# Kernel optimization log

Hardware: AMD Instinct MI355X
Metric: run time of the kernel (lower is better)

## Reference

```python
import jax, jax.numpy as jnp
import numpy as np

D_MODEL = 1024
NUM_HEADS = 16
MAX_SEQ_LEN = 2048
BATCH = 4
SEQ_LEN = 2048


def setup_inputs() -> dict:
    key = jax.random.key(0)
    ks = jax.random.split(key, 7)
    s = 0.02
    return {
        "x": jax.random.normal(ks[0], (BATCH, SEQ_LEN, D_MODEL), dtype=jnp.float32),
        "Wq": jax.random.normal(ks[1], (D_MODEL, D_MODEL), dtype=jnp.float32) * s,
        "Wk": jax.random.normal(ks[2], (D_MODEL, D_MODEL), dtype=jnp.float32) * s,
        "Wv": jax.random.normal(ks[3], (D_MODEL, D_MODEL), dtype=jnp.float32) * s,
        "Wo": jax.random.normal(ks[4], (D_MODEL, D_MODEL), dtype=jnp.float32) * s,
        "bo": jnp.zeros((D_MODEL,), dtype=jnp.float32),
        "bias_table": jax.random.normal(ks[5], (2 * MAX_SEQ_LEN - 1, NUM_HEADS), dtype=jnp.float32) * s,
    }


def reference(x, Wq, Wk, Wv, Wo, bo, bias_table):
    B, S, D = x.shape
    H = NUM_HEADS
    hd = D // H
    scale = hd ** -0.5

    # torch Linear: y = x @ W.T
    q = (x @ Wq.T).reshape(B, S, H, hd).transpose(0, 2, 1, 3)  # [B,H,S,hd]
    k = (x @ Wk.T).reshape(B, S, H, hd).transpose(0, 2, 1, 3)
    v = (x @ Wv.T).reshape(B, S, H, hd).transpose(0, 2, 1, 3)

    scores = jnp.einsum("bhqd,bhkd->bhqk", q, k) * scale  # [B,H,S,S]

    # relative index: coords[:,None] - coords[None,:] + max_seq_len - 1
    coords = jnp.arange(S)
    rel_idx = coords[:, None] - coords[None, :] + MAX_SEQ_LEN - 1  # [S,S]
    rel_bias = bias_table[rel_idx]              # [S,S,H]
    rel_bias = rel_bias.transpose(2, 0, 1)[None]  # [1,H,S,S]

    probs = jax.nn.softmax(scores + rel_bias, axis=-1)
    ctx = jnp.einsum("bhqk,bhkd->bhqd", probs, v)  # [B,H,S,hd]
    ctx = ctx.transpose(0, 2, 1, 3).reshape(B, S, D)
    return ctx @ Wo.T + bo
```

## Files before the change

### kernel.cpp

```cpp
#include <hip/hip_runtime.h>
#include <string.h>

typedef unsigned short u16;
typedef unsigned int   u32;
typedef __attribute__((ext_vector_type(8))) short short8;
typedef __attribute__((ext_vector_type(4))) float f32x4;
typedef __attribute__((ext_vector_type(16))) float f32x16;
typedef __attribute__((ext_vector_type(2))) __fp16 h2;
typedef __attribute__((ext_vector_type(8))) __fp16 h8;
typedef __attribute__((ext_vector_type(2))) unsigned int u32x2;

__device__ __forceinline__ u16 f2b(float f) {
  u32 u = __float_as_uint(f);
  u32 r = (u + 0x7fffu + ((u >> 16) & 1u)) >> 16;
  return (u16)r;
}
__device__ __forceinline__ void cp16(const u16* g, u16* l) {
  __builtin_amdgcn_global_load_lds(
      (const __attribute__((address_space(1))) void*)g,
      (__attribute__((address_space(3))) void*)l, 16, 0, 0);
}
__device__ __forceinline__ void plswap(u32& a, u32& b) {
  u32x2 r = __builtin_amdgcn_permlane32_swap(a, b, false, false);
  a = r[0]; b = r[1];
}

__global__ __launch_bounds__(256) void cvt_f2b_kernel(const float* __restrict__ in,
                                                      u16* __restrict__ out, int n) {
  int i = (blockIdx.x * 256 + threadIdx.x) * 4;
  if (i + 3 < n) {
    float4 v = *(const float4*)&in[i];
    ushort4 o = make_ushort4(f2b(v.x), f2b(v.y), f2b(v.z), f2b(v.w));
    *(ushort4*)&out[i] = o;
  }
}
__global__ __launch_bounds__(256) void cvtw_kernel(const float* __restrict__ w0,
                                                   const float* __restrict__ w1,
                                                   const float* __restrict__ w2,
                                                   const float* __restrict__ w3,
                                                   u16* __restrict__ out) {
  const float* src = (blockIdx.y == 0) ? w0 : (blockIdx.y == 1) ? w1
                   : (blockIdx.y == 2) ? w2 : w3;
  int i = (blockIdx.x * 256 + threadIdx.x) * 4;
  float4 v = *(const float4*)&src[i];
  ushort4 o = make_ushort4(f2b(v.x), f2b(v.y), f2b(v.z), f2b(v.w));
  *(ushort4*)&out[(size_t)blockIdx.y * 1048576 + i] = o;
}

template<int MODE>
__global__ __launch_bounds__(256) void gemm128_bt(
    const u16* __restrict__ A, const u16* __restrict__ Bw,
    void* __restrict__ outp, const float* __restrict__ bias,
    const int M, const int N, const int K) {
  __shared__ __attribute__((aligned(16))) u16 As[2][128 * 32];
  __shared__ __attribute__((aligned(16))) u16 Bs[2][128 * 32];

  const u16* Bw2 = Bw;
  if (MODE == 0) Bw2 += ((size_t)blockIdx.z) << 20;

  const int tid  = threadIdx.x;
  const int wave = tid >> 6, lane = tid & 63;
  const int quad = lane >> 4, l15 = lane & 15;
  const int wm   = (wave >> 1) * 64, wn = (wave & 1) * 64;
  const int m0   = blockIdx.x * 128, n0 = blockIdx.y * 128;

  const int srow = wave * 32 + (lane >> 2);
  const int scol = (lane & 3) * 8;
  const u16* gA0 = A   + (size_t)(m0 + srow) * K + scol;
  const u16* gA1 = gA0 + (size_t)16 * K;
  const u16* gB0 = Bw2 + (size_t)(n0 + srow) * K + scol;
  const u16* gB1 = gB0 + (size_t)16 * K;
  const int lo0 = (wave * 32) * 32, lo1 = (wave * 32 + 16) * 32;

  cp16(gA0, &As[0][lo0]); cp16(gA1, &As[0][lo1]);
  cp16(gB0, &Bs[0][lo0]); cp16(gB1, &Bs[0][lo1]);
  gA0 += 32; gA1 += 32; gB0 += 32; gB1 += 32;

  f32x4 acc[4][4] = {};
  const int nk = K >> 5;
  for (int kt = 0; kt < nk; ++kt) {
    const int cur = kt & 1;
    __syncthreads();
    if (kt + 1 < nk) {
      cp16(gA0, &As[1 - cur][lo0]); cp16(gA1, &As[1 - cur][lo1]);
      cp16(gB0, &Bs[1 - cur][lo0]); cp16(gB1, &Bs[1 - cur][lo1]);
      gA0 += 32; gA1 += 32; gB0 += 32; gB1 += 32;
    }
    short8 af[4], bf[4];
    #pragma unroll
    for (int mi = 0; mi < 4; ++mi)
      af[mi] = *(const short8*)&As[cur][(wm + mi * 16 + l15) * 32 + quad * 8];
    #pragma unroll
    for (int ni = 0; ni < 4; ++ni)
      bf[ni] = *(const short8*)&Bs[cur][(wn + ni * 16 + l15) * 32 + quad * 8];
    #pragma unroll
    for (int mi = 0; mi < 4; ++mi)
      #pragma unroll
      for (int ni = 0; ni < 4; ++ni)
        acc[mi][ni] = __builtin_amdgcn_mfma_f32_16x16x32_bf16(af[mi], bf[ni], acc[mi][ni], 0, 0, 0);
  }

  #pragma unroll
  for (int mi = 0; mi < 4; ++mi)
    #pragma unroll
    for (int ni = 0; ni < 4; ++ni) {
      if (MODE == 0 && blockIdx.z == 2) {
        int mb = m0 + wm + mi * 16 + quad * 4;
        int n  = n0 + wn + ni * 16 + l15;
        int b = mb >> 11, s = mb & 2047, h = n >> 6, d = n & 63;
        u16* out = (u16*)outp + (((size_t)2) << 23);
        h2 p0 = __builtin_amdgcn_cvt_pkrtz(acc[mi][ni][0], acc[mi][ni][1]);
        h2 p1 = __builtin_amdgcn_cvt_pkrtz(acc[mi][ni][2], acc[mi][ni][3]);
        ushort4 o;
        memcpy(&o.x, &p0, 4);
        memcpy(&o.z, &p1, 4);
        *(ushort4*)&out[((((size_t)b * 16 + h) * 64 + d) << 11) + s] = o;
      } else {
        #pragma unroll
        for (int r = 0; r < 4; ++r) {
          int m = m0 + wm + mi * 16 + quad * 4 + r;
          int n = n0 + wn + ni * 16 + l15;
          float v = acc[mi][ni][r];
          if (MODE == 0) {
            int b = m >> 11, s = m & 2047, h = n >> 6, d = n & 63;
            u16* out = (u16*)outp + (((size_t)blockIdx.z) << 23);
            out[((((size_t)b * 16 + h) * 2048 + s) << 6) + d] = f2b(v);
          } else {
            ((float*)outp)[(size_t)m * N + n] = v + bias[n];
          }
        }
      }
    }
}

__global__ __launch_bounds__(256, 4) void attn_mfma_kernel(
    const u16* __restrict__ qb, const u16* __restrict__ kb, const u16* __restrict__ vtb,
    const float* __restrict__ bias_table, u16* __restrict__ ctx) {
  __shared__ __attribute__((aligned(16))) u16 Ks[2][64 * 64];
  __shared__ __attribute__((aligned(16))) u16 Vs[64 * 64];
  __shared__ __attribute__((aligned(16))) float bias_s[2304];

  const int tid  = threadIdx.x;
  const int wave = tid >> 6, lane = tid & 63;
  const int l31  = lane & 31, hi = lane >> 5;
  const int xsw  = l31 & 7;
  const int bh   = blockIdx.x, h = bh & 15, b = bh >> 4;
  const int q0   = blockIdx.y * 128;

  for (int i = tid; i < 2175; i += 256)
    bias_s[i] = bias_table[(q0 + i) * 16 + h] * 1.44269504f;

  short8 aQ[4];
  #pragma unroll
  for (int ks = 0; ks < 4; ++ks)
    aQ[ks] = *(const short8*)&qb[((size_t)bh * 2048 + q0 + wave * 32 + l31) * 64
                                 + ks * 16 + hi * 8];

  f32x16 accO[2] = {};
  float  lsum = 0.f;

  const int krow = lane >> 3;
  const int kchk = (lane & 7) ^ krow;
  const u16* kbase = kb + (((size_t)bh * 2048) << 6);

  const int srow = tid >> 2, t0 = tid & 3, ssw = srow & 7;
  const u16* vrow = vtb + (((size_t)bh * 64 + srow) << 11) + t0 * 16;
  const int vo0 = srow * 64 + (((2 * t0    ) ^ ssw) << 3);
  const int vo1 = srow * 64 + (((2 * t0 + 1) ^ ssw) << 3);

  short8 vpre0 = *(const short8*)&vrow[0];
  short8 vpre1 = *(const short8*)&vrow[8];
  #pragma unroll
  for (int g = 0; g < 2; ++g)
    cp16(kbase + (size_t)(wave * 16 + g * 8 + krow) * 64 + kchk * 8,
         &Ks[0][(wave * 16 + g * 8) * 64]);

  for (int kt = 0; kt < 32; ++kt) {
    const int cur = kt & 1;
    __syncthreads();
    *(short8*)&Vs[vo0] = vpre0;
    *(short8*)&Vs[vo1] = vpre1;
    __syncthreads();
    if (kt < 31) {
      const u16* vp = vrow + ((size_t)(kt + 1) << 6);
      vpre0 = *(const short8*)&vp[0];
      vpre1 = *(const short8*)&vp[8];
      #pragma unroll
      for (int g = 0; g < 2; ++g)
        cp16(kbase + (size_t)((kt + 1) * 64 + wave * 16 + g * 8 + krow) * 64 + kchk * 8,
             &Ks[1 - cur][(wave * 16 + g * 8) * 64]);
    }

    #pragma unroll
    for (int t = 0; t < 2; ++t) {
      f32x16 accS = {};
      #pragma unroll
      for (int ks = 0; ks < 4; ++ks) {
        short8 aK = *(const short8*)&Ks[cur][(t * 32 + l31) * 64
                                            + (((ks * 2 + hi) ^ xsw) << 3)];
        accS = __builtin_amdgcn_mfma_f32_32x32x16_bf16(aK, aQ[ks], accS, 0, 0, 0);
      }

      u32 d[8];
      const int ib = wave * 32 + l31 - kt * 64 - t * 32 - 4 * hi + 2047;
      #pragma unroll
      for (int rg = 0; rg < 4; ++rg) {
        const int bb = ib - 8 * rg;
        float p0 = __builtin_amdgcn_exp2f(fmaf(accS[4 * rg + 0], 0.18033688f, bias_s[bb    ]));
        float p1 = __builtin_amdgcn_exp2f(fmaf(accS[4 * rg + 1], 0.18033688f, bias_s[bb - 1]));
        float p2 = __builtin_amdgcn_exp2f(fmaf(accS[4 * rg + 2], 0.18033688f, bias_s[bb - 2]));
        float p3 = __builtin_amdgcn_exp2f(fmaf(accS[4 * rg + 3], 0.18033688f, bias_s[bb - 3]));
        lsum += (p0 + p1) + (p2 + p3);
        h2 e0; e0[0] = (__fp16)p0; e0[1] = (__fp16)p1;
        h2 e1; e1[0] = (__fp16)p2; e1[1] = (__fp16)p3;
        memcpy(&d[2 * rg],     &e0, 4);
        memcpy(&d[2 * rg + 1], &e1, 4);
      }

      #pragma unroll
      for (int sl = 0; sl < 2; ++sl) {
        u32 F0 = d[4 * sl], F1 = d[4 * sl + 1], F2 = d[4 * sl + 2], F3 = d[4 * sl + 3];
        plswap(F0, F2);
        plswap(F1, F3);
        union { u32 w[4]; h8 v; } uf;
        uf.w[0] = F0; uf.w[1] = F1; uf.w[2] = F2; uf.w[3] = F3;
        const int ch = ((t * 2 + sl) * 2 + hi) ^ xsw;
        #pragma unroll
        for (int dt = 0; dt < 2; ++dt) {
          short8 av = *(const short8*)&Vs[(dt * 32 + l31) * 64 + (ch << 3)];
          h8 avh; memcpy(&avh, &av, 16);
          accO[dt] = __builtin_amdgcn_mfma_f32_32x32x16_f16(avh, uf.v, accO[dt], 0, 0, 0);
        }
      }
    }
  }

  const float ltot = lsum + __shfl_xor(lsum, 32);
  const float inv  = 1.0f / ltot;
  const int q = q0 + wave * 32 + l31;
  #pragma unroll
  for (int dt = 0; dt < 2; ++dt)
    #pragma unroll
    for (int rg = 0; rg < 4; ++rg) {
      ushort4 o = make_ushort4(f2b(accO[dt][4 * rg + 0] * inv), f2b(accO[dt][4 * rg + 1] * inv),
                               f2b(accO[dt][4 * rg + 2] * inv), f2b(accO[dt][4 * rg + 3] * inv));
      *(ushort4*)&ctx[((size_t)b * 2048 + q) * 1024 + h * 64 + dt * 32 + rg * 8 + hi * 4] = o;
    }
}

extern "C" void kernel_launch(void* const* d_in, const int* in_sizes, int n_in,
                              void* d_out, int out_size, void* d_ws, size_t ws_size,
                              hipStream_t stream) {
  const float* x          = (const float*)d_in[0];
  const float* Wq         = (const float*)d_in[1];
  const float* Wk         = (const float*)d_in[2];
  const float* Wv         = (const float*)d_in[3];
  const float* Wo         = (const float*)d_in[4];
  const float* bo         = (const float*)d_in[5];
  const float* bias_table = (const float*)d_in[6];
  float* out = (float*)d_out;

  char* ws = (char*)d_ws;
  u16* xb   = (u16*)(ws);
  u16* wqb  = (u16*)(ws + 16777216);
  u16* wob  = (u16*)(ws + 16777216 + 3 * 2097152);
  u16* qb   = (u16*)(ws + 25165824);
  u16* kb   = qb + 8388608;
  u16* vtb  = kb + 8388608;
  u16* ctxb = (u16*)(ws + 75497472);

  cvt_f2b_kernel<<<8192, 256, 0, stream>>>(x, xb, 8388608);
  cvtw_kernel<<<dim3(1024, 4), 256, 0, stream>>>(Wq, Wk, Wv, Wo, wqb);

  gemm128_bt<0><<<dim3(64, 8, 3), 256, 0, stream>>>(
      xb, wqb, (void*)qb, nullptr, 8192, 1024, 1024);

  attn_mfma_kernel<<<dim3(64, 16), 256, 0, stream>>>(qb, kb, vtb, bias_table, ctxb);

  gemm128_bt<1><<<dim3(64, 8), 256, 0, stream>>>(
      ctxb, wob, (void*)out, bo, 8192, 1024, 1024);
}
```

Baseline: 293.4 us.

## Process two Q sub-tiles per wave and double-buffer V in attention

Each wave now handles 64 query rows (two 32-row sub-tiles) instead of 32, so every K and V fragment read from LDS feeds twice as many MFMAs and the block covers 256 queries. V is double-buffered in shared memory, which removes one __syncthreads per key tile, and its global prefetch is moved two tiles ahead. The cost is more registers (launch bounds lowered from 4 to 2 blocks per SM) and half as many blocks (512), which may reduce occupancy and latency hiding.

After: 276.0 us. -5.9%, faster.

```diff
diff --git a/kernel.cpp b/kernel.cpp
--- a/kernel.cpp
+++ b/kernel.cpp
@@ -133,11 +133,11 @@
     }
 }
 
-__global__ __launch_bounds__(256, 4) void attn_mfma_kernel(
+__global__ __launch_bounds__(256, 2) void attn_mfma_kernel(
     const u16* __restrict__ qb, const u16* __restrict__ kb, const u16* __restrict__ vtb,
     const float* __restrict__ bias_table, u16* __restrict__ ctx) {
   __shared__ __attribute__((aligned(16))) u16 Ks[2][64 * 64];
-  __shared__ __attribute__((aligned(16))) u16 Vs[64 * 64];
+  __shared__ __attribute__((aligned(16))) u16 Vs[2][64 * 64];
   __shared__ __attribute__((aligned(16))) float bias_s[2304];
 
   const int tid  = threadIdx.x;
@@ -145,19 +145,21 @@
   const int l31  = lane & 31, hi = lane >> 5;
   const int xsw  = l31 & 7;
   const int bh   = blockIdx.x, h = bh & 15, b = bh >> 4;
-  const int q0   = blockIdx.y * 128;
-
-  for (int i = tid; i < 2175; i += 256)
+  const int q0   = blockIdx.y * 256;
+
+  for (int i = tid; i < 2303; i += 256)
     bias_s[i] = bias_table[(q0 + i) * 16 + h] * 1.44269504f;
 
-  short8 aQ[4];
+  short8 aQ[2][4];
   #pragma unroll
-  for (int ks = 0; ks < 4; ++ks)
-    aQ[ks] = *(const short8*)&qb[((size_t)bh * 2048 + q0 + wave * 32 + l31) * 64
-                                 + ks * 16 + hi * 8];
-
-  f32x16 accO[2] = {};
-  float  lsum = 0.f;
+  for (int qs = 0; qs < 2; ++qs)
+    #pragma unroll
+    for (int ks = 0; ks < 4; ++ks)
+      aQ[qs][ks] = *(const short8*)&qb[((size_t)bh * 2048 + q0 + wave * 64 + qs * 32 + l31) * 64
+                                       + ks * 16 + hi * 8];
+
+  f32x16 accO[2][2] = {};
+  float  lsum[2] = {0.f, 0.f};
 
   const int krow = lane >> 3;
   const int kchk = (lane & 7) ^ krow;
@@ -170,82 +172,102 @@
 
   short8 vpre0 = *(const short8*)&vrow[0];
   short8 vpre1 = *(const short8*)&vrow[8];
+  *(short8*)&Vs[0][vo0] = vpre0;
+  *(short8*)&Vs[0][vo1] = vpre1;
   #pragma unroll
   for (int g = 0; g < 2; ++g)
     cp16(kbase + (size_t)(wave * 16 + g * 8 + krow) * 64 + kchk * 8,
          &Ks[0][(wave * 16 + g * 8) * 64]);
+  vpre0 = *(const short8*)&vrow[64];
+  vpre1 = *(const short8*)&vrow[72];
 
   for (int kt = 0; kt < 32; ++kt) {
     const int cur = kt & 1;
     __syncthreads();
-    *(short8*)&Vs[vo0] = vpre0;
-    *(short8*)&Vs[vo1] = vpre1;
-    __syncthreads();
     if (kt < 31) {
-      const u16* vp = vrow + ((size_t)(kt + 1) << 6);
-      vpre0 = *(const short8*)&vp[0];
-      vpre1 = *(const short8*)&vp[8];
       #pragma unroll
       for (int g = 0; g < 2; ++g)
         cp16(kbase + (size_t)((kt + 1) * 64 + wave * 16 + g * 8 + krow) * 64 + kchk * 8,
              &Ks[1 - cur][(wave * 16 + g * 8) * 64]);
+      *(short8*)&Vs[1 - cur][vo0] = vpre0;
+      *(short8*)&Vs[1 - cur][vo1] = vpre1;
+      if (kt < 30) {
+        const u16* vp = vrow + ((size_t)(kt + 2) << 6);
+        vpre0 = *(const short8*)&vp[0];
+        vpre1 = *(const short8*)&vp[8];
+      }
     }
 
     #pragma unroll
     for (int t = 0; t < 2; ++t) {
-      f32x16 accS = {};
-      #pragma unroll
-      for (int ks = 0; ks < 4; ++ks) {
-        short8 aK = *(const short8*)&Ks[cur][(t * 32 + l31) * 64
-                                            + (((ks * 2 + hi) ^ xsw) << 3)];
-        accS = __builtin_amdgcn_mfma_f32_32x32x16_bf16(aK, aQ[ks], accS, 0, 0, 0);
-      }
-
-      u32 d[8];
-      const int ib = wave * 32 + l31 - kt * 64 - t * 32 - 4 * hi + 2047;
-      #pragma unroll
-      for (int rg = 0; rg < 4; ++rg) {
-        const int bb = ib - 8 * rg;
-        float p0 = __builtin_amdgcn_exp2f(fmaf(accS[4 * rg + 0], 0.18033688f, bias_s[bb    ]));
-        float p1 = __builtin_amdgcn_exp2f(fmaf(accS[4 * rg + 1], 0.18033688f, bias_s[bb - 1]));
-        float p2 = __builtin_amdgcn_exp2f(fmaf(accS[4 * rg + 2], 0.18033688f, bias_s[bb - 2]));
-        float p3 = __builtin_amdgcn_exp2f(fmaf(accS[4 * rg + 3], 0.18033688f, bias_s[bb - 3]));
-        lsum += (p0 + p1) + (p2 + p3);
-        h2 e0; e0[0] = (__fp16)p0; e0[1] = (__fp16)p1;
-        h2 e1; e1[0] = (__fp16)p2; e1[1] = (__fp16)p3;
-        memcpy(&d[2 * rg],     &e0, 4);
-        memcpy(&d[2 * rg + 1], &e1, 4);
+      short8 aK[4];
+      #pragma unroll
+      for (int ks = 0; ks < 4; ++ks)
+        aK[ks] = *(const short8*)&Ks[cur][(t * 32 + l31) * 64
+                                          + (((ks * 2 + hi) ^ xsw) << 3)];
+      f32x16 accS[2] = {};
+      #pragma unroll
+      for (int ks = 0; ks < 4; ++ks)
+        #pragma unroll
+        for (int qs = 0; qs < 2; ++qs)
+          accS[qs] = __builtin_amdgcn_mfma_f32_32x32x16_bf16(aK[ks], aQ[qs][ks], accS[qs], 0, 0, 0);
+
+      u32 d[2][8];
+      #pragma unroll
+      for (int qs = 0; qs < 2; ++qs) {
+        const int ib = wave * 64 + qs * 32 + l31 - kt * 64 - t * 32 - 4 * hi + 2047;
+        #pragma unroll
+        for (int rg = 0; rg < 4; ++rg) {
+          const int bb = ib - 8 * rg;
+          float p0 = __builtin_amdgcn_exp2f(fmaf(accS[qs][4 * rg + 0], 0.18033688f, bias_s[bb    ]));
+          float p1 = __builtin_amdgcn_exp2f(fmaf(accS[qs][4 * rg + 1], 0.18033688f, bias_s[bb - 1]));
+          float p2 = __builtin_amdgcn_exp2f(fmaf(accS[qs][4 * rg + 2], 0.18033688f, bias_s[bb - 2]));
+          float p3 = __builtin_amdgcn_exp2f(fmaf(accS[qs][4 * rg + 3], 0.18033688f, bias_s[bb - 3]));
+          lsum[qs] += (p0 + p1) + (p2 + p3);
+          h2 e0; e0[0] = (__fp16)p0; e0[1] = (__fp16)p1;
+          h2 e1; e1[0] = (__fp16)p2; e1[1] = (__fp16)p3;
+          memcpy(&d[qs][2 * rg],     &e0, 4);
+          memcpy(&d[qs][2 * rg + 1], &e1, 4);
+        }
       }
 
       #pragma unroll
       for (int sl = 0; sl < 2; ++sl) {
-        u32 F0 = d[4 * sl], F1 = d[4 * sl + 1], F2 = d[4 * sl + 2], F3 = d[4 * sl + 3];
-        plswap(F0, F2);
-        plswap(F1, F3);
-        union { u32 w[4]; h8 v; } uf;
-        uf.w[0] = F0; uf.w[1] = F1; uf.w[2] = F2; uf.w[3] = F3;
         const int ch = ((t * 2 + sl) * 2 + hi) ^ xsw;
+        short8 av0 = *(const short8*)&Vs[cur][(     l31) * 64 + (ch << 3)];
+        short8 av1 = *(const short8*)&Vs[cur][(32 + l31) * 64 + (ch << 3)];
+        h8 avh0, avh1;
+        memcpy(&avh0, &av0, 16);
+        memcpy(&avh1, &av1, 16);
         #pragma unroll
-        for (int dt = 0; dt < 2; ++dt) {
-          short8 av = *(const short8*)&Vs[(dt * 32 + l31) * 64 + (ch << 3)];
-          h8 avh; memcpy(&avh, &av, 16);
-          accO[dt] = __builtin_amdgcn_mfma_f32_32x32x16_f16(avh, uf.v, accO[dt], 0, 0, 0);
+        for (int qs = 0; qs < 2; ++qs) {
+          u32 F0 = d[qs][4 * sl], F1 = d[qs][4 * sl + 1];
+          u32 F2 = d[qs][4 * sl + 2], F3 = d[qs][4 * sl + 3];
+          plswap(F0, F2);
+          plswap(F1, F3);
+          union { u32 w[4]; h8 v; } uf;
+          uf.w[0] = F0; uf.w[1] = F1; uf.w[2] = F2; uf.w[3] = F3;
+          accO[qs][0] = __builtin_amdgcn_mfma_f32_32x32x16_f16(avh0, uf.v, accO[qs][0], 0, 0, 0);
+          accO[qs][1] = __builtin_amdgcn_mfma_f32_32x32x16_f16(avh1, uf.v, accO[qs][1], 0, 0, 0);
         }
       }
     }
   }
 
-  const float ltot = lsum + __shfl_xor(lsum, 32);
-  const float inv  = 1.0f / ltot;
-  const int q = q0 + wave * 32 + l31;
   #pragma unroll
-  for (int dt = 0; dt < 2; ++dt)
-    #pragma unroll
-    for (int rg = 0; rg < 4; ++rg) {
-      ushort4 o = make_ushort4(f2b(accO[dt][4 * rg + 0] * inv), f2b(accO[dt][4 * rg + 1] * inv),
-                               f2b(accO[dt][4 * rg + 2] * inv), f2b(accO[dt][4 * rg + 3] * inv));
-      *(ushort4*)&ctx[((size_t)b * 2048 + q) * 1024 + h * 64 + dt * 32 + rg * 8 + hi * 4] = o;
-    }
+  for (int qs = 0; qs < 2; ++qs) {
+    const float ltot = lsum[qs] + __shfl_xor(lsum[qs], 32);
+    const float inv  = 1.0f / ltot;
+    const int q = q0 + wave * 64 + qs * 32 + l31;
+    #pragma unroll
+    for (int dt = 0; dt < 2; ++dt)
+      #pragma unroll
+      for (int rg = 0; rg < 4; ++rg) {
+        ushort4 o = make_ushort4(f2b(accO[qs][dt][4 * rg + 0] * inv), f2b(accO[qs][dt][4 * rg + 1] * inv),
+                                 f2b(accO[qs][dt][4 * rg + 2] * inv), f2b(accO[qs][dt][4 * rg + 3] * inv));
+        *(ushort4*)&ctx[((size_t)b * 2048 + q) * 1024 + h * 64 + dt * 32 + rg * 8 + hi * 4] = o;
+      }
+  }
 }
 
 extern "C" void kernel_launch(void* const* d_in, const int* in_sizes, int n_in,
@@ -275,7 +297,7 @@
   gemm128_bt<0><<<dim3(64, 8, 3), 256, 0, stream>>>(
       xb, wqb, (void*)qb, nullptr, 8192, 1024, 1024);
 
-  attn_mfma_kernel<<<dim3(64, 16), 256, 0, stream>>>(qb, kb, vtb, bias_table, ctxb);
+  attn_mfma_kernel<<<dim3(64, 8), 256, 0, stream>>>(qb, kb, vtb, bias_table, ctxb);
 
   gemm128_bt<1><<<dim3(64, 8), 256, 0, stream>>>(
       ctxb, wob, (void*)out, bo, 8192, 1024, 1024);
```
